# Kernel tuning notes

Measured on AMD Instinct MI355X. Metric: run time of the kernel, lower is better.

Reference implementation:

```python
import jax, jax.numpy as jnp
import numpy as np

N_HEAD, D_MODEL, D_K, D_V = 16, 1024, 64, 64
B, L = 8, 1024
LN_EPS = 1e-5
NEG_INF = -1e9


def setup_inputs() -> dict:
    key = jax.random.key(0)
    ks = jax.random.split(key, 12)
    s = 0.02
    return {
        "q": jax.random.normal(ks[0], (B, L, D_MODEL), jnp.float32),
        "k": jax.random.normal(ks[1], (B, L, D_MODEL), jnp.float32),
        "v": jax.random.normal(ks[2], (B, L, D_MODEL), jnp.float32),
        "mask": jnp.zeros((B, L, L), dtype=bool),
        "wq": jax.random.normal(ks[3], (D_MODEL, N_HEAD * D_K), jnp.float32) * s,
        "bq": jnp.zeros((N_HEAD * D_K,), jnp.float32),
        "wk": jax.random.normal(ks[4], (D_MODEL, N_HEAD * D_K), jnp.float32) * s,
        "bk": jnp.zeros((N_HEAD * D_K,), jnp.float32),
        "wv": jax.random.normal(ks[5], (D_MODEL, N_HEAD * D_V), jnp.float32) * s,
        "bv": jnp.zeros((N_HEAD * D_V,), jnp.float32),
        "wo": jax.random.normal(ks[6], (N_HEAD * D_V, D_MODEL), jnp.float32) * s,
        "bo": jnp.zeros((D_MODEL,), jnp.float32),
        "gamma": jnp.ones((D_MODEL,), jnp.float32),
        "beta": jnp.zeros((D_MODEL,), jnp.float32),
    }


def reference(q, k, v, mask, wq, bq, wk, bk, wv, bv, wo, bo, gamma, beta):
    b, lq, _ = q.shape
    lk = k.shape[1]
    residual = q
    # separate Q/K/V projections, split heads: [b, len, h, d]
    qh = (q @ wq + bq).reshape(b, lq, N_HEAD, D_K)
    kh = (k @ wk + bk).reshape(b, lk, N_HEAD, D_K)
    vh = (v @ wv + bv).reshape(b, lk, N_HEAD, D_V)
    # scaled dot-product attention (temperature = sqrt(d_k))
    scores = jnp.einsum("bqhd,bkhd->bhqk", qh, kh) / jnp.sqrt(jnp.float32(D_K))
    scores = jnp.where(mask[:, None, :, :], NEG_INF, scores)
    attn = jax.nn.softmax(scores, axis=-1)  # [b, h, lq, lk]
    ctx = jnp.einsum("bhqk,bkhd->bqhd", attn, vh).reshape(b, lq, N_HEAD * D_V)
    # out-proj (dropout is identity in eval) + residual + LayerNorm
    out = ctx @ wo + bo + residual
    mu = out.mean(-1, keepdims=True)
    var = out.var(-1, keepdims=True)
    out = (out - mu) * jax.lax.rsqrt(var + LN_EPS) * gamma + beta
    # match original attn layout: [n_head*b, lq, lk]
    attn_flat = attn.transpose(1, 0, 2, 3).reshape(N_HEAD * b, lq, lk)
    return out, attn_flat
```

## Files before the change

### kernel.cpp

```cpp
#include <hip/hip_runtime.h>
#include <stdint.h>

static constexpr int BATCH  = 8;
static constexpr int SEQ    = 1024;
static constexpr int DMODEL = 1024;
static constexpr int NHEAD  = 16;

typedef __attribute__((ext_vector_type(8))) short sh8;
typedef __attribute__((ext_vector_type(4))) float fl4;

__device__ __forceinline__ uint16_t f2bf(float f) {
    union { float f; uint32_t u; } a; a.f = f;
    uint32_t r = a.u + 0x7FFFu + ((a.u >> 16) & 1u);
    return (uint16_t)(r >> 16);
}

__device__ __forceinline__ float b2f(uint16_t u) {
    union { uint32_t u; float f; } a; a.u = ((uint32_t)u) << 16; return a.f;
}

__device__ __forceinline__ uint32_t cvtpk(float lo, float hi) {
    uint32_t r;
    asm("v_cvt_pk_bf16_f32 %0, %1, %2" : "=v"(r) : "v"(lo), "v"(hi));
    return r;
}

__device__ __forceinline__ sh8 pack_bf8(fl4 x0, fl4 x1) {
    union { uint32_t w[4]; sh8 v; } pk;
    pk.w[0] = cvtpk(x0[0], x0[1]); pk.w[1] = cvtpk(x0[2], x0[3]);
    pk.w[2] = cvtpk(x1[0], x1[1]); pk.w[3] = cvtpk(x1[2], x1[3]);
    return pk.v;
}

__device__ __forceinline__ fl4 mfma16(sh8 a, sh8 b, fl4 c) {
    return __builtin_amdgcn_mfma_f32_16x16x32_bf16(a, b, c, 0, 0, 0);
}

__device__ __forceinline__ void gload16(const void* g, void* l) {
    __builtin_amdgcn_global_load_lds(
        (const __attribute__((address_space(1))) void*)g,
        (__attribute__((address_space(3))) void*)l, 16, 0, 0);
}

__global__ __launch_bounds__(256) void cvt3_kernel(const float* __restrict__ q,
                                                   const float* __restrict__ k,
                                                   const float* __restrict__ v,
                                                   uint16_t* __restrict__ dq,
                                                   uint16_t* __restrict__ dk,
                                                   uint16_t* __restrict__ dv) {
    const int z = blockIdx.z;
    const float* src = (z == 0) ? q : (z == 1) ? k : v;
    uint16_t* dst = (z == 0) ? dq : (z == 1) ? dk : dv;
    const int t = blockIdx.x * 256 + threadIdx.x;
    #pragma unroll
    for (int it = 0; it < 2; ++it) {
        const int i = (it * 524288 + t) * 8;
        fl4 x0 = *(const fl4*)(src + i), x1 = *(const fl4*)(src + i + 4);
        *(sh8*)(dst + i) = pack_bf8(x0, x1);
    }
}

__global__ __launch_bounds__(256) void wtrans_kernel(const float* __restrict__ wq, const float* __restrict__ wk,
                                                     const float* __restrict__ wv, const float* __restrict__ wo,
                                                     uint16_t* __restrict__ tq, uint16_t* __restrict__ tk,
                                                     uint16_t* __restrict__ tv, uint16_t* __restrict__ to) {
    __shared__ uint16_t T[64][72];
    const int z = blockIdx.z;
    const float* w = (z == 0) ? wq : (z == 1) ? wk : (z == 2) ? wv : wo;
    uint16_t* wT = (z == 0) ? tq : (z == 1) ? tk : (z == 2) ? tv : to;
    const float ws = (z == 0) ? 0.125f : 1.f;
    const int n0 = blockIdx.x * 64, k0 = blockIdx.y * 64;
    const int tid = threadIdx.x;
    #pragma unroll
    for (int it = 0; it < 4; ++it) {
        int g = it * 256 + tid;
        int r = g >> 4, c = (g & 15) * 4;
        fl4 x = *(const fl4*)(w + (size_t)(k0 + r) * DMODEL + n0 + c);
        T[r][c + 0] = f2bf(x[0] * ws); T[r][c + 1] = f2bf(x[1] * ws);
        T[r][c + 2] = f2bf(x[2] * ws); T[r][c + 3] = f2bf(x[3] * ws);
    }
    __syncthreads();
    #pragma unroll
    for (int it = 0; it < 4; ++it) {
        int g = it * 256 + tid;
        int r = g >> 4, c = (g & 15) * 4;
        ushort4 o;
        o.x = T[c + 0][r]; o.y = T[c + 1][r]; o.z = T[c + 2][r]; o.w = T[c + 3][r];
        *(ushort4*)(wT + (size_t)(n0 + r) * DMODEL + k0 + c) = o;
    }
}

__global__ __launch_bounds__(256) void vtrans_kernel(const uint16_t* __restrict__ vh,
                                                     uint16_t* __restrict__ vT) {
    __shared__ uint16_t T[64][72];
    const int l0 = blockIdx.x * 64, hd0 = blockIdx.y * 64, bb = blockIdx.z;
    const uint16_t* src = vh + (size_t)bb * SEQ * DMODEL;
    uint16_t* dst = vT + (size_t)bb * SEQ * DMODEL;
    const int tid = threadIdx.x;
    #pragma unroll
    for (int it = 0; it < 4; ++it) {
        int g = it * 256 + tid;
        int r = g >> 4, c = (g & 15) * 4;
        ushort4 x = *(const ushort4*)(src + (size_t)(l0 + r) * DMODEL + hd0 + c);
        T[r][c + 0] = x.x; T[r][c + 1] = x.y; T[r][c + 2] = x.z; T[r][c + 3] = x.w;
    }
    __syncthreads();
    #pragma unroll
    for (int it = 0; it < 4; ++it) {
        int g = it * 256 + tid;
        int r = g >> 4, c = (g & 15) * 4;
        ushort4 o;
        o.x = T[c + 0][r]; o.y = T[c + 1][r]; o.z = T[c + 2][r]; o.w = T[c + 3][r];
        *(ushort4*)(dst + (size_t)(hd0 + r) * DMODEL + l0 + c) = o;
    }
}

template<bool OUT_BF16, bool RESID>
__device__ __forceinline__
void gemm_body(const uint16_t* __restrict__ Ab, const uint16_t* __restrict__ Bt,
               const float* __restrict__ bias, float bscale, const float* __restrict__ resid,
               void* __restrict__ Cv, int m0, int n0,
               uint16_t* Alds, uint16_t* Blds) {
    const int tid = threadIdx.x;
    const int lane = tid & 63, wid = tid >> 6;
    const int wr = (wid >> 1) * 64, wc = (wid & 1) * 64;
    const int fr = lane & 15, fk = (lane >> 4) * 8;

    fl4 acc[4][4];
    #pragma unroll
    for (int i = 0; i < 4; ++i)
        #pragma unroll
        for (int j = 0; j < 4; ++j) acc[i][j] = (fl4){0.f, 0.f, 0.f, 0.f};

    for (int kt = 0; kt < 16; ++kt) {
        const int kb = kt * 64;
        #pragma unroll
        for (int it = 0; it < 4; ++it) {
            const int g = it * 256 + tid;
            const int r = g >> 3, c = (g & 7) << 3;
            const int lofs = __builtin_amdgcn_readfirstlane((it * 256 + wid * 64) * 16);
            gload16(Ab + (size_t)(m0 + r) * DMODEL + kb + c, (char*)Alds + lofs);
            gload16(Bt + (size_t)(n0 + r) * DMODEL + kb + c, (char*)Blds + lofs);
        }
        __syncthreads();
        #pragma unroll
        for (int ks = 0; ks < 2; ++ks) {
            sh8 a[4], bb[4];
            #pragma unroll
            for (int mi = 0; mi < 4; ++mi) a[mi] = *(const sh8*)&Alds[(wr + mi * 16 + fr) * 64 + ks * 32 + fk];
            #pragma unroll
            for (int ni = 0; ni < 4; ++ni) bb[ni] = *(const sh8*)&Blds[(wc + ni * 16 + fr) * 64 + ks * 32 + fk];
            #pragma unroll
            for (int mi = 0; mi < 4; ++mi)
                #pragma unroll
                for (int ni = 0; ni < 4; ++ni) acc[mi][ni] = mfma16(a[mi], bb[ni], acc[mi][ni]);
        }
        __syncthreads();
    }

    #pragma unroll
    for (int mi = 0; mi < 4; ++mi) {
        #pragma unroll
        for (int ni = 0; ni < 4; ++ni) {
            const int col = n0 + wc + ni * 16 + fr;
            const float bv = bias[col] * bscale;
            #pragma unroll
            for (int i = 0; i < 4; ++i) {
                const int row = m0 + wr + mi * 16 + (lane >> 4) * 4 + i;
                float val = acc[mi][ni][i] + bv;
                if (RESID) val += resid[(size_t)row * DMODEL + col];
                if (OUT_BF16) ((uint16_t*)Cv)[(size_t)row * DMODEL + col] = f2bf(val);
                else          ((float*)Cv)[(size_t)row * DMODEL + col] = val;
            }
        }
    }
}

__global__ __launch_bounds__(256)
void gemm_proj(const uint16_t* __restrict__ A0, const uint16_t* __restrict__ A1, const uint16_t* __restrict__ A2,
               const uint16_t* __restrict__ B0, const uint16_t* __restrict__ B1, const uint16_t* __restrict__ B2,
               const float* __restrict__ b0, const float* __restrict__ b1, const float* __restrict__ b2,
               uint16_t* __restrict__ C0, uint16_t* __restrict__ C1, uint16_t* __restrict__ C2) {
    __shared__ uint16_t Alds[128 * 64];
    __shared__ uint16_t Blds[128 * 64];
    const int z = blockIdx.z;
    const uint16_t* Ab = (z == 0) ? A0 : (z == 1) ? A1 : A2;
    const uint16_t* Bt = (z == 0) ? B0 : (z == 1) ? B1 : B2;
    const float* bias  = (z == 0) ? b0 : (z == 1) ? b1 : b2;
    uint16_t* Cv       = (z == 0) ? C0 : (z == 1) ? C1 : C2;
    const float bs     = (z == 0) ? 0.125f : 1.f;
    gemm_body<true, false>(Ab, Bt, bias, bs, nullptr, Cv, blockIdx.x * 128, blockIdx.y * 128, Alds, Blds);
}

__global__ __launch_bounds__(256)
void gemm_out(const uint16_t* __restrict__ Ab, const uint16_t* __restrict__ Bt,
              const float* __restrict__ bias, const float* __restrict__ resid,
              float* __restrict__ Cv) {
    __shared__ uint16_t Alds[128 * 64];
    __shared__ uint16_t Blds[128 * 64];
    gemm_body<false, true>(Ab, Bt, bias, 1.f, resid, Cv, blockIdx.x * 128, blockIdx.y * 128, Alds, Blds);
}

__global__ __launch_bounds__(256)
void attn_kernel(const uint16_t* __restrict__ qh, const uint16_t* __restrict__ kh,
                 const uint16_t* __restrict__ vT, const uint8_t* __restrict__ mask,
                 float* __restrict__ attn, uint16_t* __restrict__ ctx) {
    __shared__ uint16_t S[16 * 1024];
    __shared__ float rinv[16];
    const int b = blockIdx.x, h = blockIdx.y, q0 = blockIdx.z * 16;
    const int tid = threadIdx.x, lane = tid & 63, wid = tid >> 6;
    const int fr = lane & 15, fk = (lane >> 4) * 8, frow4 = (lane >> 4) * 4;

    sh8 Aq[2];
    #pragma unroll
    for (int ks = 0; ks < 2; ++ks)
        Aq[ks] = *(const sh8*)(qh + (size_t)(b * SEQ + q0 + fr) * DMODEL + h * 64 + ks * 32 + fk);

    for (int t8 = 0; t8 < 8; ++t8) {
        const int kv0 = (t8 * 4 + wid) * 32;
        sh8 Bk[2][2];
        #pragma unroll
        for (int ni = 0; ni < 2; ++ni)
            #pragma unroll
            for (int ks = 0; ks < 2; ++ks)
                Bk[ni][ks] = *(const sh8*)(kh + (size_t)(b * SEQ + kv0 + ni * 16 + fr) * DMODEL + h * 64 + ks * 32 + fk);
        fl4 sa[2];
        #pragma unroll
        for (int ni = 0; ni < 2; ++ni) sa[ni] = (fl4){0.f, 0.f, 0.f, 0.f};
        #pragma unroll
        for (int ni = 0; ni < 2; ++ni)
            #pragma unroll
            for (int ks = 0; ks < 2; ++ks) sa[ni] = mfma16(Aq[ks], Bk[ni][ks], sa[ni]);
        #pragma unroll
        for (int ni = 0; ni < 2; ++ni)
            #pragma unroll
            for (int i = 0; i < 4; ++i) {
                const int row = frow4 + i, col = kv0 + ni * 16 + fr;
                S[row * 1024 + ((((col >> 3) ^ (row & 15)) << 3) | (col & 7))] = f2bf(sa[ni][i]);
            }
    }
    __syncthreads();

    {
        const int r = tid >> 4, j = tid & 15;
        const int rbase = r * 1024;
        const uint8_t* mbase = mask + (size_t)(b * SEQ + q0 + r) * SEQ;
        sh8 x[8];
        uint2 mw[8];
        float mx = -1e30f;
        #pragma unroll
        for (int c4 = 0; c4 < 8; ++c4) {
            const int cc = c4 * 16 + j;
            x[c4] = *(sh8*)&S[rbase + ((cc ^ r) << 3)];
            mw[c4] = *(const uint2*)(mbase + cc * 8);
            #pragma unroll
            for (int t = 0; t < 4; ++t) {
                float f = ((mw[c4].x >> (t * 8)) & 0xFF) ? -1e9f : b2f((uint16_t)x[c4][t]);
                mx = fmaxf(mx, f);
            }
            #pragma unroll
            for (int t = 0; t < 4; ++t) {
                float f = ((mw[c4].y >> (t * 8)) & 0xFF) ? -1e9f : b2f((uint16_t)x[c4][4 + t]);
                mx = fmaxf(mx, f);
            }
        }
        #pragma unroll
        for (int d = 1; d < 16; d <<= 1) mx = fmaxf(mx, __shfl_xor(mx, d));
        float sum = 0.f;
        sh8 sv[8];
        #pragma unroll
        for (int c4 = 0; c4 < 8; ++c4) {
            const int cc = c4 * 16 + j;
            float e[8];
            #pragma unroll
            for (int t = 0; t < 4; ++t) {
                float f = ((mw[c4].x >> (t * 8)) & 0xFF) ? -1e9f : b2f((uint16_t)x[c4][t]);
                e[t] = __expf(f - mx);
            }
            #pragma unroll
            for (int t = 0; t < 4; ++t) {
                float f = ((mw[c4].y >> (t * 8)) & 0xFF) ? -1e9f : b2f((uint16_t)x[c4][4 + t]);
                e[4 + t] = __expf(f - mx);
            }
            union { uint32_t w[4]; sh8 v; } pk;
            pk.w[0] = cvtpk(e[0], e[1]); pk.w[1] = cvtpk(e[2], e[3]);
            pk.w[2] = cvtpk(e[4], e[5]); pk.w[3] = cvtpk(e[6], e[7]);
            sv[c4] = pk.v;
            *(sh8*)&S[rbase + ((cc ^ r) << 3)] = pk.v;
            sum += e[0] + e[1] + e[2] + e[3] + e[4] + e[5] + e[6] + e[7];
        }
        #pragma unroll
        for (int d = 1; d < 16; d <<= 1) sum += __shfl_xor(sum, d);
        const float ri = 1.f / sum;
        if (j == 0) rinv[r] = ri;
        float* ab = attn + ((size_t)((h * BATCH + b) * SEQ + q0 + r)) * SEQ;
        #pragma unroll
        for (int c4 = 0; c4 < 8; ++c4) {
            const int cc = c4 * 16 + j;
            fl4 o0, o1;
            #pragma unroll
            for (int t = 0; t < 4; ++t) o0[t] = b2f((uint16_t)sv[c4][t]) * ri;
            #pragma unroll
            for (int t = 0; t < 4; ++t) o1[t] = b2f((uint16_t)sv[c4][4 + t]) * ri;
            float* dst = ab + cc * 8;
            __builtin_nontemporal_store(o0, (fl4*)dst);
            __builtin_nontemporal_store(o1, (fl4*)(dst + 4));
        }
    }
    __syncthreads();

    fl4 acc0 = (fl4){0.f, 0.f, 0.f, 0.f}, acc1 = (fl4){0.f, 0.f, 0.f, 0.f};
    const uint16_t* vbase = vT + (size_t)((b * NHEAD + h) * 64 + wid * 16) * SEQ;
    const int frx = fr & 15;
    #pragma unroll 4
    for (int ks2 = 0; ks2 < 32; ++ks2) {
        const int kv = ks2 * 32;
        sh8 Ap = *(const sh8*)&S[fr * 1024 + ((((kv + fk) >> 3) ^ frx) << 3)];
        sh8 Bv = *(const sh8*)(vbase + (size_t)fr * SEQ + kv + fk);
        if (ks2 & 1) acc1 = mfma16(Ap, Bv, acc1);
        else         acc0 = mfma16(Ap, Bv, acc0);
    }
    #pragma unroll
    for (int i = 0; i < 4; ++i) {
        const int q = frow4 + i;
        const float val = (acc0[i] + acc1[i]) * rinv[q];
        ctx[(size_t)(b * SEQ + q0 + q) * DMODEL + h * 64 + wid * 16 + fr] = f2bf(val);
    }
}

__global__ __launch_bounds__(256)
void ln_kernel(const float* __restrict__ raw, const float* __restrict__ gamma,
               const float* __restrict__ beta, float* __restrict__ out) {
    const int row = blockIdx.x;
    const int tid = threadIdx.x;
    const float* x = raw + (size_t)row * DMODEL;
    fl4 xv = *(const fl4*)(x + tid * 4);
    float s  = xv[0] + xv[1] + xv[2] + xv[3];
    float ss = xv[0] * xv[0] + xv[1] * xv[1] + xv[2] * xv[2] + xv[3] * xv[3];
    #pragma unroll
    for (int d = 1; d < 64; d <<= 1) { s += __shfl_xor(s, d); ss += __shfl_xor(ss, d); }
    __shared__ float sb[4], ssb[4];
    if ((tid & 63) == 0) { sb[tid >> 6] = s; ssb[tid >> 6] = ss; }
    __syncthreads();
    s  = sb[0] + sb[1] + sb[2] + sb[3];
    ss = ssb[0] + ssb[1] + ssb[2] + ssb[3];
    const float mu  = s * (1.f / 1024.f);
    const float var = ss * (1.f / 1024.f) - mu * mu;
    const float rstd = rsqrtf(var + 1e-5f);
    fl4 g  = *(const fl4*)(gamma + tid * 4);
    fl4 be = *(const fl4*)(beta + tid * 4);
    fl4 o;
    #pragma unroll
    for (int j = 0; j < 4; ++j) o[j] = (xv[j] - mu) * rstd * g[j] + be[j];
    *(fl4*)(out + (size_t)row * DMODEL + tid * 4) = o;
}

extern "C" void kernel_launch(void* const* d_in, const int* in_sizes, int n_in,
                              void* d_out, int out_size, void* d_ws, size_t ws_size,
                              hipStream_t stream) {
    (void)in_sizes; (void)n_in; (void)out_size; (void)ws_size;
    const float* q     = (const float*)d_in[0];
    const float* k     = (const float*)d_in[1];
    const float* v     = (const float*)d_in[2];
    const uint8_t* mask = (const uint8_t*)d_in[3];
    const float* wq = (const float*)d_in[4];
    const float* bq = (const float*)d_in[5];
    const float* wk = (const float*)d_in[6];
    const float* bk = (const float*)d_in[7];
    const float* wv = (const float*)d_in[8];
    const float* bv = (const float*)d_in[9];
    const float* wo = (const float*)d_in[10];
    const float* bo = (const float*)d_in[11];
    const float* gamma = (const float*)d_in[12];
    const float* beta  = (const float*)d_in[13];

    float* out  = (float*)d_out;
    float* attn = out + (size_t)BATCH * SEQ * DMODEL;

    uint16_t* qcvt = (uint16_t*)(attn);
    uint16_t* kcvt = (uint16_t*)((char*)attn + ((size_t)16 << 20));
    uint16_t* vcvt = (uint16_t*)((char*)attn + ((size_t)32 << 20));

    char* ws = (char*)d_ws;
    uint16_t* qh   = (uint16_t*)(ws);
    uint16_t* kh   = (uint16_t*)(ws + ((size_t)16 << 20));
    uint16_t* vT   = (uint16_t*)(ws + ((size_t)32 << 20));
    uint16_t* ctx  = (uint16_t*)(ws + ((size_t)48 << 20));
    uint16_t* wqT  = (uint16_t*)(ws + ((size_t)64 << 20));
    uint16_t* wkT  = (uint16_t*)(ws + ((size_t)66 << 20));
    uint16_t* wvT  = (uint16_t*)(ws + ((size_t)68 << 20));
    uint16_t* woT  = (uint16_t*)(ws + ((size_t)70 << 20));
    uint16_t* vtmp = (uint16_t*)(ws + ((size_t)72 << 20));

    dim3 tb(256);
    wtrans_kernel<<<dim3(16, 16, 4), tb, 0, stream>>>(wq, wk, wv, wo, wqT, wkT, wvT, woT);
    cvt3_kernel<<<dim3(2048, 1, 3), tb, 0, stream>>>(q, k, v, qcvt, kcvt, vcvt);

    gemm_proj<<<dim3(64, 8, 3), tb, 0, stream>>>(qcvt, kcvt, vcvt, wqT, wkT, wvT,
                                                 bq, bk, bv, qh, kh, vtmp);

    vtrans_kernel<<<dim3(16, 16, 8), tb, 0, stream>>>(vtmp, vT);

    attn_kernel<<<dim3(BATCH, NHEAD, 64), tb, 0, stream>>>(qh, kh, vT, mask, attn, ctx);

    gemm_out<<<dim3(64, 8), tb, 0, stream>>>(ctx, woT, bo, q, out);

    ln_kernel<<<BATCH * SEQ, tb, 0, stream>>>(out, gamma, beta, out);
}
```

Before: 455.2 us.

## Merge prep kernels, stage GEMM epilogues through LDS, coalesce attn-prob stores

The weight-transpose and input-conversion kernels are merged into one launch. Both GEMM epilogues now stage results in swizzled LDS and write full 16-byte rows, replacing scattered scalar stores. The attention kernel moves the fp32 probability write to after the PV loop and reads the bf16 tile from LDS so each thread writes contiguous fl4 chunks. This should cut uncoalesced global writes and one launch, at the cost of extra LDS traffic and barriers.

```diff
diff --git a/kernel.cpp b/kernel.cpp
--- a/kernel.cpp
+++ b/kernel.cpp
@@ -42,51 +42,50 @@
         (__attribute__((address_space(3))) void*)l, 16, 0, 0);
 }
 
-__global__ __launch_bounds__(256) void cvt3_kernel(const float* __restrict__ q,
-                                                   const float* __restrict__ k,
+__global__ __launch_bounds__(256) void prep_kernel(const float* __restrict__ wq, const float* __restrict__ wk,
+                                                   const float* __restrict__ wv, const float* __restrict__ wo,
+                                                   uint16_t* __restrict__ tq, uint16_t* __restrict__ tk,
+                                                   uint16_t* __restrict__ tv, uint16_t* __restrict__ to,
+                                                   const float* __restrict__ q, const float* __restrict__ k,
                                                    const float* __restrict__ v,
-                                                   uint16_t* __restrict__ dq,
-                                                   uint16_t* __restrict__ dk,
+                                                   uint16_t* __restrict__ dq, uint16_t* __restrict__ dk,
                                                    uint16_t* __restrict__ dv) {
-    const int z = blockIdx.z;
-    const float* src = (z == 0) ? q : (z == 1) ? k : v;
-    uint16_t* dst = (z == 0) ? dq : (z == 1) ? dk : dv;
-    const int t = blockIdx.x * 256 + threadIdx.x;
-    #pragma unroll
-    for (int it = 0; it < 2; ++it) {
-        const int i = (it * 524288 + t) * 8;
-        fl4 x0 = *(const fl4*)(src + i), x1 = *(const fl4*)(src + i + 4);
-        *(sh8*)(dst + i) = pack_bf8(x0, x1);
-    }
-}
-
-__global__ __launch_bounds__(256) void wtrans_kernel(const float* __restrict__ wq, const float* __restrict__ wk,
-                                                     const float* __restrict__ wv, const float* __restrict__ wo,
-                                                     uint16_t* __restrict__ tq, uint16_t* __restrict__ tk,
-                                                     uint16_t* __restrict__ tv, uint16_t* __restrict__ to) {
     __shared__ uint16_t T[64][72];
     const int z = blockIdx.z;
-    const float* w = (z == 0) ? wq : (z == 1) ? wk : (z == 2) ? wv : wo;
-    uint16_t* wT = (z == 0) ? tq : (z == 1) ? tk : (z == 2) ? tv : to;
-    const float ws = (z == 0) ? 0.125f : 1.f;
-    const int n0 = blockIdx.x * 64, k0 = blockIdx.y * 64;
     const int tid = threadIdx.x;
-    #pragma unroll
-    for (int it = 0; it < 4; ++it) {
-        int g = it * 256 + tid;
-        int r = g >> 4, c = (g & 15) * 4;
-        fl4 x = *(const fl4*)(w + (size_t)(k0 + r) * DMODEL + n0 + c);
-        T[r][c + 0] = f2bf(x[0] * ws); T[r][c + 1] = f2bf(x[1] * ws);
-        T[r][c + 2] = f2bf(x[2] * ws); T[r][c + 3] = f2bf(x[3] * ws);
-    }
-    __syncthreads();
-    #pragma unroll
-    for (int it = 0; it < 4; ++it) {
-        int g = it * 256 + tid;
-        int r = g >> 4, c = (g & 15) * 4;
-        ushort4 o;
-        o.x = T[c + 0][r]; o.y = T[c + 1][r]; o.z = T[c + 2][r]; o.w = T[c + 3][r];
-        *(ushort4*)(wT + (size_t)(n0 + r) * DMODEL + k0 + c) = o;
+    if (z < 4) {
+        const float* w = (z == 0) ? wq : (z == 1) ? wk : (z == 2) ? wv : wo;
+        uint16_t* wT = (z == 0) ? tq : (z == 1) ? tk : (z == 2) ? tv : to;
+        const float ws = (z == 0) ? 0.125f : 1.f;
+        const int n0 = blockIdx.x * 64, k0 = blockIdx.y * 64;
+        #pragma unroll
+        for (int it = 0; it < 4; ++it) {
+            int g = it * 256 + tid;
+            int r = g >> 4, c = (g & 15) * 4;
+            fl4 x = *(const fl4*)(w + (size_t)(k0 + r) * DMODEL + n0 + c);
+            T[r][c + 0] = f2bf(x[0] * ws); T[r][c + 1] = f2bf(x[1] * ws);
+            T[r][c + 2] = f2bf(x[2] * ws); T[r][c + 3] = f2bf(x[3] * ws);
+        }
+        __syncthreads();
+        #pragma unroll
+        for (int it = 0; it < 4; ++it) {
+            int g = it * 256 + tid;
+            int r = g >> 4, c = (g & 15) * 4;
+            ushort4 o;
+            o.x = T[c + 0][r]; o.y = T[c + 1][r]; o.z = T[c + 2][r]; o.w = T[c + 3][r];
+            *(ushort4*)(wT + (size_t)(n0 + r) * DMODEL + k0 + c) = o;
+        }
+    } else {
+        const int zz = z - 4;
+        const float* src = (zz == 0) ? q : (zz == 1) ? k : v;
+        uint16_t* dst = (zz == 0) ? dq : (zz == 1) ? dk : dv;
+        const int bid = blockIdx.y * 16 + blockIdx.x;
+        #pragma unroll
+        for (int it = 0; it < 16; ++it) {
+            const size_t i = ((size_t)bid * 4096 + it * 256 + tid) * 8;
+            fl4 x0 = *(const fl4*)(src + i), x1 = *(const fl4*)(src + i + 4);
+            *(sh8*)(dst + i) = pack_bf8(x0, x1);
+        }
     }
 }
 
@@ -119,12 +118,13 @@
 __device__ __forceinline__
 void gemm_body(const uint16_t* __restrict__ Ab, const uint16_t* __restrict__ Bt,
                const float* __restrict__ bias, float bscale, const float* __restrict__ resid,
-               void* __restrict__ Cv, int m0, int n0,
-               uint16_t* Alds, uint16_t* Blds) {
+               void* __restrict__ Cv, int m0, int n0, uint16_t* lds) {
+    uint16_t* Alds = lds;
+    uint16_t* Blds = lds + 128 * 64;
     const int tid = threadIdx.x;
     const int lane = tid & 63, wid = tid >> 6;
     const int wr = (wid >> 1) * 64, wc = (wid & 1) * 64;
-    const int fr = lane & 15, fk = (lane >> 4) * 8;
+    const int fr = lane & 15, fk = (lane >> 4) * 8, frow4 = (lane >> 4) * 4;
 
     fl4 acc[4][4];
     #pragma unroll
@@ -158,19 +158,62 @@
         __syncthreads();
     }
 
-    #pragma unroll
-    for (int mi = 0; mi < 4; ++mi) {
-        #pragma unroll
-        for (int ni = 0; ni < 4; ++ni) {
-            const int col = n0 + wc + ni * 16 + fr;
-            const float bv = bias[col] * bscale;
-            #pragma unroll
-            for (int i = 0; i < 4; ++i) {
-                const int row = m0 + wr + mi * 16 + (lane >> 4) * 4 + i;
-                float val = acc[mi][ni][i] + bv;
-                if (RESID) val += resid[(size_t)row * DMODEL + col];
-                if (OUT_BF16) ((uint16_t*)Cv)[(size_t)row * DMODEL + col] = f2bf(val);
-                else          ((float*)Cv)[(size_t)row * DMODEL + col] = val;
+    if (OUT_BF16) {
+        #pragma unroll
+        for (int mi = 0; mi < 4; ++mi) {
+            #pragma unroll
+            for (int ni = 0; ni < 4; ++ni) {
+                const int col = wc + ni * 16 + fr;
+                const float bv = bias[n0 + col] * bscale;
+                #pragma unroll
+                for (int i = 0; i < 4; ++i) {
+                    const int row = wr + mi * 16 + frow4 + i;
+                    lds[row * 128 + ((((col >> 3) ^ (row & 7)) << 3) | (col & 7))] = f2bf(acc[mi][ni][i] + bv);
+                }
+            }
+        }
+        __syncthreads();
+        #pragma unroll
+        for (int it = 0; it < 8; ++it) {
+            const int ch = it * 256 + tid;
+            const int row = ch >> 4, cc = ch & 15;
+            sh8 vv = *(sh8*)&lds[row * 128 + ((cc ^ (row & 7)) << 3)];
+            *(sh8*)((uint16_t*)Cv + (size_t)(m0 + row) * DMODEL + n0 + cc * 8) = vv;
+        }
+    } else {
+        float* flds = (float*)lds;
+        #pragma unroll
+        for (int h2 = 0; h2 < 2; ++h2) {
+            if (h2) __syncthreads();
+            if (wc == h2 * 64) {
+                #pragma unroll
+                for (int ni = 0; ni < 4; ++ni) {
+                    const int col = wc + ni * 16 + fr;
+                    const int ch = col - h2 * 64;
+                    const float bv = bias[n0 + col] * bscale;
+                    #pragma unroll
+                    for (int i = 0; i < 4; ++i) {
+                        const int row = wr + (0) * 16 + frow4 + i; (void)row;
+                    }
+                    #pragma unroll
+                    for (int mi = 0; mi < 4; ++mi) {
+                        #pragma unroll
+                        for (int i = 0; i < 4; ++i) {
+                            const int row = wr + mi * 16 + frow4 + i;
+                            float val = acc[mi][ni][i] + bv;
+                            if (RESID) val += resid[(size_t)(m0 + row) * DMODEL + n0 + col];
+                            flds[row * 64 + ((((ch >> 2) ^ (row & 7)) << 2) | (ch & 3))] = val;
+                        }
+                    }
+                }
+            }
+            __syncthreads();
+            #pragma unroll
+            for (int it = 0; it < 8; ++it) {
+                const int ck = it * 256 + tid;
+                const int row = ck >> 4, cc = ck & 15;
+                fl4 vv = *(fl4*)&flds[row * 64 + ((cc ^ (row & 7)) << 2)];
+                *(fl4*)((float*)Cv + (size_t)(m0 + row) * DMODEL + n0 + h2 * 64 + cc * 4) = vv;
             }
         }
     }
@@ -181,24 +224,22 @@
                const uint16_t* __restrict__ B0, const uint16_t* __restrict__ B1, const uint16_t* __restrict__ B2,
                const float* __restrict__ b0, const float* __restrict__ b1, const float* __restrict__ b2,
                uint16_t* __restrict__ C0, uint16_t* __restrict__ C1, uint16_t* __restrict__ C2) {
-    __shared__ uint16_t Alds[128 * 64];
-    __shared__ uint16_t Blds[128 * 64];
+    __shared__ uint16_t lds[2 * 128 * 64];
     const int z = blockIdx.z;
     const uint16_t* Ab = (z == 0) ? A0 : (z == 1) ? A1 : A2;
     const uint16_t* Bt = (z == 0) ? B0 : (z == 1) ? B1 : B2;
     const float* bias  = (z == 0) ? b0 : (z == 1) ? b1 : b2;
     uint16_t* Cv       = (z == 0) ? C0 : (z == 1) ? C1 : C2;
     const float bs     = (z == 0) ? 0.125f : 1.f;
-    gemm_body<true, false>(Ab, Bt, bias, bs, nullptr, Cv, blockIdx.x * 128, blockIdx.y * 128, Alds, Blds);
+    gemm_body<true, false>(Ab, Bt, bias, bs, nullptr, Cv, blockIdx.x * 128, blockIdx.y * 128, lds);
 }
 
 __global__ __launch_bounds__(256)
 void gemm_out(const uint16_t* __restrict__ Ab, const uint16_t* __restrict__ Bt,
               const float* __restrict__ bias, const float* __restrict__ resid,
               float* __restrict__ Cv) {
-    __shared__ uint16_t Alds[128 * 64];
-    __shared__ uint16_t Blds[128 * 64];
-    gemm_body<false, true>(Ab, Bt, bias, 1.f, resid, Cv, blockIdx.x * 128, blockIdx.y * 128, Alds, Blds);
+    __shared__ uint16_t lds[2 * 128 * 64];
+    gemm_body<false, true>(Ab, Bt, bias, 1.f, resid, Cv, blockIdx.x * 128, blockIdx.y * 128, lds);
 }
 
 __global__ __launch_bounds__(256)
@@ -267,7 +308,6 @@
         #pragma unroll
         for (int d = 1; d < 16; d <<= 1) mx = fmaxf(mx, __shfl_xor(mx, d));
         float sum = 0.f;
-        sh8 sv[8];
         #pragma unroll
         for (int c4 = 0; c4 < 8; ++c4) {
             const int cc = c4 * 16 + j;
@@ -285,37 +325,21 @@
             union { uint32_t w[4]; sh8 v; } pk;
             pk.w[0] = cvtpk(e[0], e[1]); pk.w[1] = cvtpk(e[2], e[3]);
             pk.w[2] = cvtpk(e[4], e[5]); pk.w[3] = cvtpk(e[6], e[7]);
-            sv[c4] = pk.v;
             *(sh8*)&S[rbase + ((cc ^ r) << 3)] = pk.v;
             sum += e[0] + e[1] + e[2] + e[3] + e[4] + e[5] + e[6] + e[7];
         }
         #pragma unroll
         for (int d = 1; d < 16; d <<= 1) sum += __shfl_xor(sum, d);
-        const float ri = 1.f / sum;
-        if (j == 0) rinv[r] = ri;
-        float* ab = attn + ((size_t)((h * BATCH + b) * SEQ + q0 + r)) * SEQ;
-        #pragma unroll
-        for (int c4 = 0; c4 < 8; ++c4) {
-            const int cc = c4 * 16 + j;
-            fl4 o0, o1;
-            #pragma unroll
-            for (int t = 0; t < 4; ++t) o0[t] = b2f((uint16_t)sv[c4][t]) * ri;
-            #pragma unroll
-            for (int t = 0; t < 4; ++t) o1[t] = b2f((uint16_t)sv[c4][4 + t]) * ri;
-            float* dst = ab + cc * 8;
-            __builtin_nontemporal_store(o0, (fl4*)dst);
-            __builtin_nontemporal_store(o1, (fl4*)(dst + 4));
-        }
+        if (j == 0) rinv[r] = 1.f / sum;
     }
     __syncthreads();
 
     fl4 acc0 = (fl4){0.f, 0.f, 0.f, 0.f}, acc1 = (fl4){0.f, 0.f, 0.f, 0.f};
     const uint16_t* vbase = vT + (size_t)((b * NHEAD + h) * 64 + wid * 16) * SEQ;
-    const int frx = fr & 15;
     #pragma unroll 4
     for (int ks2 = 0; ks2 < 32; ++ks2) {
         const int kv = ks2 * 32;
-        sh8 Ap = *(const sh8*)&S[fr * 1024 + ((((kv + fk) >> 3) ^ frx) << 3)];
+        sh8 Ap = *(const sh8*)&S[fr * 1024 + ((((kv + fk) >> 3) ^ fr) << 3)];
         sh8 Bv = *(const sh8*)(vbase + (size_t)fr * SEQ + kv + fk);
         if (ks2 & 1) acc1 = mfma16(Ap, Bv, acc1);
         else         acc0 = mfma16(Ap, Bv, acc0);
@@ -325,6 +349,22 @@
         const int q = frow4 + i;
         const float val = (acc0[i] + acc1[i]) * rinv[q];
         ctx[(size_t)(b * SEQ + q0 + q) * DMODEL + h * 64 + wid * 16 + fr] = f2bf(val);
+    }
+
+    {
+        float* ab = attn + ((size_t)((h * BATCH + b) * SEQ + q0)) * SEQ;
+        #pragma unroll
+        for (int it = 0; it < 16; ++it) {
+            const int ch = it * 256 + tid;
+            const int row = ch >> 8, oc = ch & 255;
+            const int cc = oc >> 1, half = oc & 1;
+            const ushort4 p = *(const ushort4*)&S[row * 1024 + ((cc ^ row) << 3) + half * 4];
+            const float ri = rinv[row];
+            fl4 o;
+            o[0] = b2f(p.x) * ri; o[1] = b2f(p.y) * ri;
+            o[2] = b2f(p.z) * ri; o[3] = b2f(p.w) * ri;
+            __builtin_nontemporal_store(o, (fl4*)(ab + (size_t)ch * 4));
+        }
     }
 }
 
@@ -393,8 +433,8 @@
     uint16_t* vtmp = (uint16_t*)(ws + ((size_t)72 << 20));
 
     dim3 tb(256);
-    wtrans_kernel<<<dim3(16, 16, 4), tb, 0, stream>>>(wq, wk, wv, wo, wqT, wkT, wvT, woT);
-    cvt3_kernel<<<dim3(2048, 1, 3), tb, 0, stream>>>(q, k, v, qcvt, kcvt, vcvt);
+    prep_kernel<<<dim3(16, 16, 7), tb, 0, stream>>>(wq, wk, wv, wo, wqT, wkT, wvT, woT,
+                                                    q, k, v, qcvt, kcvt, vcvt);
 
     gemm_proj<<<dim3(64, 8, 3), tb, 0, stream>>>(qcvt, kcvt, vcvt, wqT, wkT, wvT,
                                                  bq, bk, bv, qh, kh, vtmp);
```

Measured after the change: 449.1 us. Within noise of the previous version (-1.3%).
